# Optimization experiments

Hardware: AMD Instinct MI355X
Metric: run time of the kernel (lower is better)

## Reference

```python
import jax, jax.numpy as jnp
import numpy as np

# ---- config (mirrors init_kwargs) ----
T = 1024          # num tokens (one causal sequence)
H = 1024          # hidden_size
NQ, NK, D = 16, 4, 64   # q heads, kv heads, head_dim (GQA)
I_DENSE = 4096    # dense FFN intermediate
I_MOE = 512       # expert FFN intermediate
E, K = 8, 2       # num_experts, top_k
EPS = 1e-6
THETA = 10000.0


def setup_inputs() -> dict:
    key = jax.random.key(0)
    ks = jax.random.split(key, 20)
    rn = lambda k, shp: (jax.random.normal(k, shp, dtype=jnp.float32) * 0.02)
    QKV = (NQ + 2 * NK) * D
    return {
        "hidden_states": jax.random.normal(ks[0], (T, H), dtype=jnp.float32),
        "residual": jax.random.normal(ks[1], (T, H), dtype=jnp.float32),
        "positions": jnp.arange(T, dtype=jnp.int32),
        "ln0_w": jnp.ones((H,), jnp.float32),
        "pa0_w": jnp.ones((H,), jnp.float32),
        "ln1_w": jnp.ones((H,), jnp.float32),
        "pa1_w": jnp.ones((H,), jnp.float32),
        # attention weights (stored [in, out] so x @ W)
        "qkv0_w": rn(ks[2], (H, QKV)),
        "o0_w": rn(ks[3], (NQ * D, H)),
        "qkv1_w": rn(ks[4], (H, QKV)),
        "o1_w": rn(ks[5], (NQ * D, H)),
        # dense MLPs (merged gate_up: first half gate, second half up)
        "gu0_w": rn(ks[6], (H, 2 * I_DENSE)),
        "dn0_w": rn(ks[7], (I_DENSE, H)),
        "gu1_w": rn(ks[8], (H, 2 * I_DENSE)),
        "dn1_w": rn(ks[9], (I_DENSE, H)),
        # MoE: router gate + per-expert SwiGLU weights
        "gate_w": rn(ks[10], (H, E)),
        "w13": rn(ks[11], (E, H, 2 * I_MOE)),
        "w2": rn(ks[12], (E, I_MOE, H)),
    }


def _rmsnorm(x, w):
    v = jnp.mean(jnp.square(x.astype(jnp.float32)), axis=-1, keepdims=True)
    return (x.astype(jnp.float32) * jax.lax.rsqrt(v + EPS)).astype(x.dtype) * w


def _add_rmsnorm(x, res, w):
    # sglang fused add + RMSNorm: residual <- x + residual; out <- rmsnorm(residual)
    res = x + res
    return _rmsnorm(res, w), res


def _rope(pos, x):
    # neox-style rotary over full head_dim; x: [T, n_heads, D]
    half = D // 2
    inv_freq = 1.0 / (THETA ** (jnp.arange(half, dtype=jnp.float32) / half))
    f = pos.astype(jnp.float32)[:, None] * inv_freq            # [T, half]
    cos, sin = jnp.cos(f)[:, None, :], jnp.sin(f)[:, None, :]  # [T, 1, half]
    x1, x2 = x[..., :half], x[..., half:]
    return jnp.concatenate([x1 * cos - x2 * sin, x2 * cos + x1 * sin], axis=-1)


def _attention(pos, x, qkv_w, o_w):
    qkv = x @ qkv_w
    q = qkv[:, : NQ * D].reshape(T, NQ, D)
    k = qkv[:, NQ * D : (NQ + NK) * D].reshape(T, NK, D)
    v = qkv[:, (NQ + NK) * D :].reshape(T, NK, D)
    q, k = _rope(pos, q), _rope(pos, k)
    g = NQ // NK
    qg = q.reshape(T, NK, g, D)
    scores = jnp.einsum("tkgd,skd->kgts", qg, k) * (D ** -0.5)  # [NK,g,T,T]
    causal = jnp.tril(jnp.ones((T, T), bool))
    scores = jnp.where(causal, scores, jnp.float32(-1e30))
    p = jax.nn.softmax(scores, axis=-1)
    o = jnp.einsum("kgts,skd->tkgd", p, v).reshape(T, NQ * D)
    return o @ o_w


def _dense_mlp(x, gu_w, dn_w):
    gu = x @ gu_w
    h = jax.nn.silu(gu[:, :I_DENSE]) * gu[:, I_DENSE:]  # SiluAndMul
    return h @ dn_w


def _moe(x, gate_w, w13, w2):
    # router in fp32 (router_dtype == 'float32'), softmax, top-k, no renormalize
    logits = x.astype(jnp.float32) @ gate_w.astype(jnp.float32)  # [T, E]
    probs = jax.nn.softmax(logits, axis=-1)
    topw, topi = jax.lax.top_k(probs, K)                         # [T, K]
    rows = jnp.arange(x.shape[0])[:, None]
    combine = jnp.zeros((x.shape[0], E), jnp.float32).at[rows, topi].set(topw)
    combine = combine.astype(x.dtype)
    out = jnp.zeros_like(x)
    for e in range(E):  # fixed small expert count: grouped-GEMM reference
        g = x @ w13[e]
        h = jax.nn.silu(g[:, :I_MOE]) * g[:, I_MOE:]
        out = out + combine[:, e : e + 1] * (h @ w2[e])
    return out


def reference(hidden_states, residual, positions, ln0_w, pa0_w, ln1_w, pa1_w,
              qkv0_w, o0_w, qkv1_w, o1_w, gu0_w, dn0_w, gu1_w, dn1_w,
              gate_w, w13, w2):
    h, r = _add_rmsnorm(hidden_states, residual, ln0_w)
    h = _attention(positions, h, qkv0_w, o0_w)
    h, r = _add_rmsnorm(h, r, pa0_w)
    shortcut = _moe(h, gate_w, w13, w2)      # MoE runs on the shortcut branch
    h = _dense_mlp(h, gu0_w, dn0_w)
    h, r = _add_rmsnorm(h, r, ln1_w)
    h = _attention(positions, h, qkv1_w, o1_w)
    h, r = _add_rmsnorm(h, r, pa1_w)
    h = _dense_mlp(h, gu1_w, dn1_w)
    h = h + shortcut                          # combine shortcut MoE output
    return h, r
```

## Files before the change

### kernel.cpp

```cpp
#include <hip/hip_runtime.h>
#include <math.h>

namespace {

constexpr int kT = 1024;
constexpr int kH = 1024;
constexpr int kNQ = 16;
constexpr int kNKV = 4;
constexpr int kD = 64;
constexpr int kQKV = (kNQ + 2 * kNKV) * kD;
constexpr int kIDense = 4096;
constexpr int kIMoe = 512;
constexpr int kE = 8;
constexpr float kEps = 1e-6f;

typedef __attribute__((ext_vector_type(8))) short short8;
typedef __attribute__((ext_vector_type(4))) float f32x4;

__device__ __forceinline__ ushort f2bf(float f) {
    union { float f; uint32_t u; } v; v.f = f;
    uint32_t r = (v.u + 0x7fffu + ((v.u >> 16) & 1u)) >> 16;
    return (ushort)r;
}
__device__ __forceinline__ float f4el(const float4& v, int i) {
    return (i == 0) ? v.x : (i == 1) ? v.y : (i == 2) ? v.z : v.w;
}
__device__ __forceinline__ void gload16(const void* g, void* l) {
    __builtin_amdgcn_global_load_lds(
        (const __attribute__((address_space(1))) void*)g,
        (__attribute__((address_space(3))) void*)l, 16, 0, 0);
}

__global__ __launch_bounds__(256) void add_rmsnorm_kernel(
    const float* __restrict__ x, const float* __restrict__ res,
    const float* __restrict__ w, float* __restrict__ h32,
    ushort* __restrict__ h16, float* __restrict__ r_out)
{
    __shared__ float red[4];
    const int t = blockIdx.x;
    const int i = threadIdx.x;
    const size_t base = (size_t)t * kH;
    float4 a = reinterpret_cast<const float4*>(x + base)[i];
    float4 b = reinterpret_cast<const float4*>(res + base)[i];
    float4 s = make_float4(a.x + b.x, a.y + b.y, a.z + b.z, a.w + b.w);
    reinterpret_cast<float4*>(r_out + base)[i] = s;
    float ss = s.x * s.x + s.y * s.y + s.z * s.z + s.w * s.w;
    #pragma unroll
    for (int off = 32; off > 0; off >>= 1) ss += __shfl_down(ss, off);
    if ((i & 63) == 0) red[i >> 6] = ss;
    __syncthreads();
    const float tot = red[0] + red[1] + red[2] + red[3];
    const float inv = rsqrtf(tot * (1.0f / kH) + kEps);
    float4 wv = reinterpret_cast<const float4*>(w)[i];
    float4 o = make_float4(s.x * inv * wv.x, s.y * inv * wv.y,
                           s.z * inv * wv.z, s.w * inv * wv.w);
    reinterpret_cast<float4*>(h32 + base)[i] = o;
    ushort4 u;
    u.x = f2bf(o.x); u.y = f2bf(o.y); u.z = f2bf(o.z); u.w = f2bf(o.w);
    reinterpret_cast<ushort4*>(h16 + base)[i] = u;
}

__global__ __launch_bounds__(256) void transpose_bf16_kernel(
    const float* __restrict__ W, ushort* __restrict__ WT,
    int R, int Cn, int ld_w, long w_z_stride, long wt_z_stride)
{
    __shared__ float tile[64][65];
    const int z = blockIdx.z;
    const float* Wz = W + (size_t)z * w_z_stride;
    ushort* WTz = WT + (size_t)z * wt_z_stride;
    const int r0 = blockIdx.y * 64;
    const int c0 = blockIdx.x * 64;
    const int tr = threadIdx.x >> 4;
    const int tc4 = (threadIdx.x & 15) * 4;
    #pragma unroll
    for (int p = 0; p < 4; p++) {
        float4 v = *reinterpret_cast<const float4*>(
            &Wz[(size_t)(r0 + p * 16 + tr) * ld_w + c0 + tc4]);
        tile[p * 16 + tr][tc4 + 0] = v.x;
        tile[p * 16 + tr][tc4 + 1] = v.y;
        tile[p * 16 + tr][tc4 + 2] = v.z;
        tile[p * 16 + tr][tc4 + 3] = v.w;
    }
    __syncthreads();
    #pragma unroll
    for (int p = 0; p < 4; p++) {
        const int oc = p * 16 + tr;
        ushort4 u;
        u.x = f2bf(tile[tc4 + 0][oc]);
        u.y = f2bf(tile[tc4 + 1][oc]);
        u.z = f2bf(tile[tc4 + 2][oc]);
        u.w = f2bf(tile[tc4 + 3][oc]);
        *reinterpret_cast<ushort4*>(&WTz[(size_t)(c0 + oc) * R + r0 + tc4]) = u;
    }
}

template <bool GATED>
__global__ __launch_bounds__(256) void mgemm_kernel(
    const ushort* __restrict__ A, const float* __restrict__ B,
    float* __restrict__ Cf, ushort* __restrict__ C16,
    const float* __restrict__ scale,
    int lda, int ldb, int ldc, int kc,
    int gate_off_cols, long b_z_stride, int c_z_col, int k_z_off,
    int scale_stride, int atomic_flag)
{
    __shared__ __align__(16) ushort As[64 * 64];
    __shared__ __align__(16) ushort Bs[64 * 72];
    __shared__ __align__(16) ushort Us[GATED ? 64 * 72 : 8];

    const int z = blockIdx.z;
    const int m0 = blockIdx.y * 64;
    const int n0 = blockIdx.x * 64;
    const int tid = threadIdx.x;
    const float* Bz = B + (size_t)z * b_z_stride;
    const int k0 = z * k_z_off;

    const int arow = tid >> 3;
    const int achk = tid & 7;
    const int bt = tid & 15;
    const int bq = tid >> 4;

    const int lane = tid & 63;
    const int wave = tid >> 6;
    const int wr = (wave >> 1) * 32;
    const int wc = (wave & 1) * 32;
    const int lrow = lane & 15;
    const int lg = lane >> 4;

    f32x4 accg[2][2] = {};
    f32x4 accu[2][2] = {};

    for (int kk0 = 0; kk0 < kc; kk0 += 64) {
        const int kbase = k0 + kk0;
        #pragma unroll
        for (int c = 0; c < 2; c++) {
            const int row = c * 32 + arow;
            const int cs = (achk + (row & 7)) & 7;
            gload16(A + (size_t)(m0 + row) * lda + kbase + cs * 8,
                    (char*)As + c * 4096 + tid * 16);
        }
        #pragma unroll
        for (int p = 0; p < 2; p++) {
            const int kp = bq + p * 16;
            const long krow = (long)(kbase + kp * 2) * ldb + n0 + bt * 4;
            float4 b0 = *reinterpret_cast<const float4*>(Bz + krow);
            float4 b1 = *reinterpret_cast<const float4*>(Bz + krow + ldb);
            float4 u0, u1;
            if constexpr (GATED) {
                u0 = *reinterpret_cast<const float4*>(Bz + krow + gate_off_cols);
                u1 = *reinterpret_cast<const float4*>(Bz + krow + ldb + gate_off_cols);
            }
            #pragma unroll
            for (int i = 0; i < 4; i++) {
                const int n = bt * 4 + i;
                const int ld = (kp + 4 * ((n >> 2) & 7)) & 31;
                uint32_t pk = (uint32_t)f2bf(f4el(b0, i)) |
                              ((uint32_t)f2bf(f4el(b1, i)) << 16);
                *reinterpret_cast<uint32_t*>(&Bs[n * 72 + ld * 2]) = pk;
                if constexpr (GATED) {
                    uint32_t pu = (uint32_t)f2bf(f4el(u0, i)) |
                                  ((uint32_t)f2bf(f4el(u1, i)) << 16);
                    *reinterpret_cast<uint32_t*>(&Us[n * 72 + ld * 2]) = pu;
                }
            }
        }
        __syncthreads();

        short8 af[2][2], bfr[2][2];
        #pragma unroll
        for (int mf = 0; mf < 2; mf++)
            #pragma unroll
            for (int kk = 0; kk < 2; kk++) {
                const int r = wr + mf * 16 + lrow;
                const int ch = kk * 4 + lg;
                const int sl = (ch - (r & 7)) & 7;
                af[mf][kk] = *reinterpret_cast<const short8*>(
                    (const char*)As + r * 128 + sl * 16);
            }
        #pragma unroll
        for (int nf = 0; nf < 2; nf++)
            #pragma unroll
            for (int kk = 0; kk < 2; kk++) {
                const int n = wc + nf * 16 + lrow;
                const int ldd = ((kk * 16 + lg * 4) + 4 * ((n >> 2) & 7)) & 31;
                bfr[nf][kk] = *reinterpret_cast<const short8*>(&Bs[n * 72 + ldd * 2]);
            }
        #pragma unroll
        for (int mf = 0; mf < 2; mf++)
            #pragma unroll
            for (int nf = 0; nf < 2; nf++)
                #pragma unroll
                for (int kk = 0; kk < 2; kk++)
                    accg[mf][nf] = __builtin_amdgcn_mfma_f32_16x16x32_bf16(
                        af[mf][kk], bfr[nf][kk], accg[mf][nf], 0, 0, 0);
        if constexpr (GATED) {
            short8 uf[2][2];
            #pragma unroll
            for (int nf = 0; nf < 2; nf++)
                #pragma unroll
                for (int kk = 0; kk < 2; kk++) {
                    const int n = wc + nf * 16 + lrow;
                    const int ldd = ((kk * 16 + lg * 4) + 4 * ((n >> 2) & 7)) & 31;
                    uf[nf][kk] = *reinterpret_cast<const short8*>(&Us[n * 72 + ldd * 2]);
                }
            #pragma unroll
            for (int mf = 0; mf < 2; mf++)
                #pragma unroll
                for (int nf = 0; nf < 2; nf++)
                    #pragma unroll
                    for (int kk = 0; kk < 2; kk++)
                        accu[mf][nf] = __builtin_amdgcn_mfma_f32_16x16x32_bf16(
                            af[mf][kk], uf[nf][kk], accu[mf][nf], 0, 0, 0);
        }
        __syncthreads();
    }

    const int r4 = (lane >> 4) * 4;
    const int cl = lane & 15;
    const int ccol = z * c_z_col;
    #pragma unroll
    for (int mf = 0; mf < 2; mf++) {
        #pragma unroll
        for (int nf = 0; nf < 2; nf++) {
            #pragma unroll
            for (int j = 0; j < 4; j++) {
                const int row = m0 + wr + mf * 16 + r4 + j;
                const int col = ccol + n0 + wc + nf * 16 + cl;
                if constexpr (GATED) {
                    const float g = accg[mf][nf][j];
                    const float u = accu[mf][nf][j];
                    const float sv =
                        scale ? scale[(size_t)row * scale_stride + z] : 1.0f;
                    const float h = (g / (1.0f + __expf(-g))) * u * sv;
                    C16[(size_t)row * ldc + col] = f2bf(h);
                } else if (atomic_flag) {
                    atomicAdd(&Cf[(size_t)row * ldc + col], accg[mf][nf][j]);
                } else {
                    Cf[(size_t)row * ldc + col] = accg[mf][nf][j];
                }
            }
        }
    }
}

__global__ __launch_bounds__(256) void rope_pack_kernel(
    const float* __restrict__ qkv, const int* __restrict__ positions,
    ushort* __restrict__ Qb, ushort* __restrict__ Kb)
{
    const int t = blockIdx.x;
    const float pos = (float)positions[t];
    for (int item = threadIdx.x; item < (kNQ + kNKV) * 32; item += 256) {
        const int head = item >> 5;
        const int i = item & 31;
        const float inv_freq = powf(10000.0f, -(float)i * (1.0f / 32.0f));
        const float f = pos * inv_freq;
        float sv, cv;
        sincosf(f, &sv, &cv);
        const size_t off = (size_t)t * kQKV + head * kD;
        const float x1 = qkv[off + i];
        const float x2 = qkv[off + 32 + i];
        const float r1 = x1 * cv - x2 * sv;
        const float r2 = x2 * cv + x1 * sv;
        if (head < kNQ) {
            ushort* q = Qb + ((size_t)head * kT + t) * kD;
            q[i] = f2bf(r1 * 0.125f);
            q[i + 32] = f2bf(r2 * 0.125f);
        } else {
            ushort* k = Kb + ((size_t)(head - kNQ) * kT + t) * kD;
            k[i] = f2bf(r1);
            k[i + 32] = f2bf(r2);
        }
    }
}

__global__ __launch_bounds__(64) void gate_topk_kernel(
    const float* __restrict__ h, const float* __restrict__ gate_w,
    float* __restrict__ combine)
{
    const int t = blockIdx.x;
    const int lane = threadIdx.x;
    float acc[kE] = {};
    for (int i = lane; i < kH; i += 64) {
        const float xv = h[(size_t)t * kH + i];
        const float* gw = gate_w + (size_t)i * kE;
        #pragma unroll
        for (int e = 0; e < kE; e++) acc[e] += xv * gw[e];
    }
    #pragma unroll
    for (int e = 0; e < kE; e++) {
        #pragma unroll
        for (int off = 32; off > 0; off >>= 1) acc[e] += __shfl_down(acc[e], off);
    }
    if (lane == 0) {
        float mx = acc[0];
        #pragma unroll
        for (int e = 1; e < kE; e++) mx = fmaxf(mx, acc[e]);
        float p[kE];
        float s = 0.0f;
        #pragma unroll
        for (int e = 0; e < kE; e++) { p[e] = expf(acc[e] - mx); s += p[e]; }
        const float invs = 1.0f / s;
        #pragma unroll
        for (int e = 0; e < kE; e++) p[e] *= invs;
        int i1 = 0;
        #pragma unroll
        for (int e = 1; e < kE; e++) if (p[e] > p[i1]) i1 = e;
        int i2 = (i1 == 0) ? 1 : 0;
        #pragma unroll
        for (int e = 0; e < kE; e++) if (e != i1 && p[e] > p[i2]) i2 = e;
        float outv[kE];
        #pragma unroll
        for (int e = 0; e < kE; e++) outv[e] = 0.0f;
        outv[i1] = p[i1];
        outv[i2] = p[i2];
        #pragma unroll
        for (int e = 0; e < kE; e++) combine[(size_t)t * kE + e] = outv[e];
    }
}

__global__ __launch_bounds__(256) void attn_mfma_kernel(
    const ushort* __restrict__ Qb, const ushort* __restrict__ Kb,
    const ushort* __restrict__ Vt, ushort* __restrict__ attn_o)
{
    __shared__ __align__(16) ushort Qs[64 * 64];
    __shared__ __align__(16) ushort Ks[64 * 64];
    __shared__ __align__(16) ushort Vs[64 * 64];
    __shared__ __align__(16) ushort Ps[64 * 64];
    const int tid = threadIdx.x;
    const int qb = blockIdx.x * 64;
    const int hq = blockIdx.y;
    const int kvh = hq >> 2;
    const int lane = tid & 63;
    const int wave = tid >> 6;
    const int lrow = lane & 15;
    const int g = lane >> 4;
    const int srow = tid >> 3;
    const int sx = tid & 7;
    const ushort* Qg = Qb + ((size_t)hq * kT + qb) * kD;
    const ushort* Kg = Kb + (size_t)kvh * kT * kD;
    const ushort* Vg = Vt + (size_t)kvh * kD * kT;
    const int xr = (lrow & 7) << 4;

    #pragma unroll
    for (int c = 0; c < 2; c++) {
        const int row = c * 32 + srow;
        gload16(Qg + (size_t)row * kD + ((sx ^ (row & 7)) * 8),
                (char*)Qs + c * 4096 + tid * 16);
    }
    __syncthreads();
    short8 qf[2];
    #pragma unroll
    for (int kk = 0; kk < 2; kk++)
        qf[kk] = *reinterpret_cast<const short8*>(
            (const char*)Qs + (16 * wave + lrow) * 128 + ((kk * 64 + g * 16) ^ xr));

    f32x4 oacc[4] = {};
    float mrow = -1e30f, lsum = 0.0f;

    for (int s0 = 0; s0 <= qb; s0 += 64) {
        __syncthreads();
        #pragma unroll
        for (int c = 0; c < 2; c++) {
            const int row = c * 32 + srow;
            gload16(Kg + (size_t)(s0 + row) * kD + ((sx ^ (row & 7)) * 8),
                    (char*)Ks + c * 4096 + tid * 16);
            gload16(Vg + (size_t)row * kT + s0 + ((sx ^ (row & 7)) * 8),
                    (char*)Vs + c * 4096 + tid * 16);
        }
        __syncthreads();

        f32x4 sacc[4] = {};
        #pragma unroll
        for (int nf = 0; nf < 4; nf++) {
            #pragma unroll
            for (int kk = 0; kk < 2; kk++) {
                short8 kf = *reinterpret_cast<const short8*>(
                    (const char*)Ks + (nf * 16 + lrow) * 128 + ((kk * 64 + g * 16) ^ xr));
                sacc[nf] = __builtin_amdgcn_mfma_f32_16x16x32_bf16(
                    kf, qf[kk], sacc[nf], 0, 0, 0);
            }
        }

        const bool diag = (s0 == qb);
        float pv[16];
        float mloc = -1e30f;
        #pragma unroll
        for (int nf = 0; nf < 4; nf++)
            #pragma unroll
            for (int j = 0; j < 4; j++) {
                float s = sacc[nf][j];
                if (diag && (nf * 16 + g * 4 + j > 16 * wave + lrow)) s = -1e30f;
                pv[nf * 4 + j] = s;
                mloc = fmaxf(mloc, s);
            }
        mloc = fmaxf(mloc, __shfl_xor(mloc, 16));
        mloc = fmaxf(mloc, __shfl_xor(mloc, 32));
        const float mnew = fmaxf(mrow, mloc);
        const float alpha = __expf(mrow - mnew);
        float psum = 0.0f;
        #pragma unroll
        for (int j = 0; j < 16; j++) { pv[j] = __expf(pv[j] - mnew); psum += pv[j]; }
        psum += __shfl_xor(psum, 16);
        psum += __shfl_xor(psum, 32);
        lsum = lsum * alpha + psum;
        mrow = mnew;

        const int prow = 16 * wave + lrow;
        #pragma unroll
        for (int nf = 0; nf < 4; nf++)
            #pragma unroll
            for (int jp = 0; jp < 2; jp++) {
                uint32_t pk = (uint32_t)f2bf(pv[nf * 4 + jp * 2]) |
                              ((uint32_t)f2bf(pv[nf * 4 + jp * 2 + 1]) << 16);
                *reinterpret_cast<uint32_t*>(
                    (char*)Ps + prow * 128 + ((nf * 32 + g * 8 + jp * 4) ^ xr)) = pk;
            }

        float aj[4];
        #pragma unroll
        for (int j = 0; j < 4; j++) aj[j] = __shfl(alpha, g * 4 + j);
        #pragma unroll
        for (int nf = 0; nf < 4; nf++)
            #pragma unroll
            for (int j = 0; j < 4; j++) oacc[nf][j] *= aj[j];

        short8 paf[2];
        #pragma unroll
        for (int kk = 0; kk < 2; kk++)
            paf[kk] = *reinterpret_cast<const short8*>(
                (const char*)Ps + prow * 128 + ((kk * 64 + g * 16) ^ xr));
        #pragma unroll
        for (int nf = 0; nf < 4; nf++)
            #pragma unroll
            for (int kk = 0; kk < 2; kk++) {
                short8 vf = *reinterpret_cast<const short8*>(
                    (const char*)Vs + (nf * 16 + lrow) * 128 + ((kk * 64 + g * 16) ^ xr));
                oacc[nf] = __builtin_amdgcn_mfma_f32_16x16x32_bf16(
                    paf[kk], vf, oacc[nf], 0, 0, 0);
            }
    }

    float lj[4];
    #pragma unroll
    for (int j = 0; j < 4; j++) lj[j] = 1.0f / __shfl(lsum, g * 4 + j);
    #pragma unroll
    for (int nf = 0; nf < 4; nf++)
        #pragma unroll
        for (int j = 0; j < 4; j++) {
            const int trow = qb + 16 * wave + g * 4 + j;
            attn_o[(size_t)trow * (kNQ * kD) + hq * kD + nf * 16 + lrow] =
                f2bf(oacc[nf][j] * lj[j]);
        }
}

__global__ __launch_bounds__(256) void final_out_kernel(
    const float* __restrict__ mlp, const float* __restrict__ shortcut,
    const float* __restrict__ r, float* __restrict__ out)
{
    const int i = blockIdx.x * 256 + threadIdx.x;
    float4 a = reinterpret_cast<const float4*>(mlp)[i];
    float4 b = reinterpret_cast<const float4*>(shortcut)[i];
    reinterpret_cast<float4*>(out)[i] =
        make_float4(a.x + b.x, a.y + b.y, a.z + b.z, a.w + b.w);
    reinterpret_cast<float4*>(out + (size_t)kT * kH)[i] =
        reinterpret_cast<const float4*>(r)[i];
}

}

extern "C" void kernel_launch(void* const* d_in, const int* in_sizes, int n_in,
                              void* d_out, int out_size, void* d_ws, size_t ws_size,
                              hipStream_t stream) {
    (void)in_sizes; (void)n_in; (void)out_size; (void)ws_size;
    const float* hidden   = (const float*)d_in[0];
    const float* residual = (const float*)d_in[1];
    const int*   positions= (const int*)d_in[2];
    const float* ln0_w    = (const float*)d_in[3];
    const float* pa0_w    = (const float*)d_in[4];
    const float* ln1_w    = (const float*)d_in[5];
    const float* pa1_w    = (const float*)d_in[6];
    const float* qkv0_w   = (const float*)d_in[7];
    const float* o0_w     = (const float*)d_in[8];
    const float* qkv1_w   = (const float*)d_in[9];
    const float* o1_w     = (const float*)d_in[10];
    const float* gu0_w    = (const float*)d_in[11];
    const float* dn0_w    = (const float*)d_in[12];
    const float* gu1_w    = (const float*)d_in[13];
    const float* dn1_w    = (const float*)d_in[14];
    const float* gate_w   = (const float*)d_in[15];
    const float* w13      = (const float*)d_in[16];
    const float* w2       = (const float*)d_in[17];
    float* out_h = (float*)d_out;

    char* wsb = (char*)d_ws;
    float*  r_buf   = (float*)(wsb + (0ull  << 20));
    float*  h32     = (float*)(wsb + (4ull  << 20));
    float*  t0_buf  = (float*)(wsb + (8ull  << 20));
    float*  qkv_buf = (float*)(wsb + (12ull << 20));
    float*  sc_buf  = (float*)(wsb + (18ull << 20));
    float*  cb_buf  = (float*)(wsb + (22ull << 20));
    ushort* h16     = (ushort*)(wsb + (23ull << 20));
    ushort* ao16    = (ushort*)(wsb + (25ull << 20));
    ushort* he16    = (ushort*)(wsb + (27ull << 20));
    ushort* Qb      = (ushort*)(wsb + (35ull << 20));
    ushort* Kb      = (ushort*)(wsb + (37ull << 20));
    ushort* VtG     = (ushort*)(wsb + (38ull << 20));

    auto gemm_f32 = [&](const ushort* A, const float* B, float* C, int N,
                        int lda_, int ldb_, int ldc_, int nz, int kc, int kzoff,
                        int atomic) {
        mgemm_kernel<false><<<dim3(N / 64, kT / 64, nz), 256, 0, stream>>>(
            A, B, C, nullptr, nullptr, lda_, ldb_, ldc_, kc,
            0, 0, 0, kzoff, 0, atomic);
    };
    auto attention = [&](const float* qkv_w, const float* o_w) {
        gemm_f32(h16, qkv_w, qkv_buf, kQKV, kH, kQKV, kQKV, 1, kH, 0, 0);
        rope_pack_kernel<<<kT, 256, 0, stream>>>(qkv_buf, positions, Qb, Kb);
        transpose_bf16_kernel<<<dim3(1, kT / 64, kNKV), 256, 0, stream>>>(
            qkv_buf + (kNQ + kNKV) * kD, VtG, kT, kD, kQKV, kD, (long)kD * kT);
        attn_mfma_kernel<<<dim3(kT / 64, kNQ), 256, 0, stream>>>(Qb, Kb, VtG, ao16);
        hipMemsetAsync(t0_buf, 0, (size_t)kT * kH * 4, stream);
        gemm_f32(ao16, o_w, t0_buf, kH, kNQ * kD, kH, kH, 2, 512, 512, 1);
    };
    auto dense_mlp = [&](const float* gu_w, const float* dn_w) {
        mgemm_kernel<true><<<dim3(kIDense / 64, kT / 64, 1), 256, 0, stream>>>(
            h16, gu_w, nullptr, he16, nullptr, kH, 2 * kIDense, kIDense, kH,
            kIDense, 0, 0, 0, 0, 0);
        hipMemsetAsync(t0_buf, 0, (size_t)kT * kH * 4, stream);
        gemm_f32(he16, dn_w, t0_buf, kH, kIDense, kH, kH, 4, 1024, 1024, 1);
    };

    add_rmsnorm_kernel<<<kT, 256, 0, stream>>>(hidden, residual, ln0_w, h32, h16, r_buf);
    attention(qkv0_w, o0_w);
    add_rmsnorm_kernel<<<kT, 256, 0, stream>>>(t0_buf, r_buf, pa0_w, h32, h16, r_buf);
    gate_topk_kernel<<<kT, 64, 0, stream>>>(h32, gate_w, cb_buf);
    mgemm_kernel<true><<<dim3(kIMoe / 64, kT / 64, kE), 256, 0, stream>>>(
        h16, w13, nullptr, he16, cb_buf, kH, 2 * kIMoe, kIDense, kH,
        kIMoe, (long)kH * 2 * kIMoe, kIMoe, 0, kE, 0);
    hipMemsetAsync(sc_buf, 0, (size_t)kT * kH * 4, stream);
    gemm_f32(he16, w2, sc_buf, kH, kIDense, kH, kH, 4, 1024, 1024, 1);
    dense_mlp(gu0_w, dn0_w);
    add_rmsnorm_kernel<<<kT, 256, 0, stream>>>(t0_buf, r_buf, ln1_w, h32, h16, r_buf);
    attention(qkv1_w, o1_w);
    add_rmsnorm_kernel<<<kT, 256, 0, stream>>>(t0_buf, r_buf, pa1_w, h32, h16, r_buf);
    dense_mlp(gu1_w, dn1_w);
    final_out_kernel<<<(kT * kH / 4) / 256, 256, 0, stream>>>(t0_buf, sc_buf, r_buf, out_h);
}
```

Measured before the change: 390.5 us.

## Double-buffer shared-memory tiles in mgemm to overlap loads with MFMA

Shared-memory A/B/U tiles in the GEMM kernel are now double-buffered. The next K-tile's A async load and B global loads into registers are issued before the current tile's MFMAs, and the B conversion is written to the alternate buffer afterwards. This hides global-load latency behind compute and drops one barrier per iteration. In exchange it doubles LDS use, which may lower occupancy, and adds register pressure from holding B prefetch data across the MFMA section.

```diff
diff --git a/kernel.cpp b/kernel.cpp
--- a/kernel.cpp
+++ b/kernel.cpp
@@ -103,9 +103,9 @@
     int gate_off_cols, long b_z_stride, int c_z_col, int k_z_off,
     int scale_stride, int atomic_flag)
 {
-    __shared__ __align__(16) ushort As[64 * 64];
-    __shared__ __align__(16) ushort Bs[64 * 72];
-    __shared__ __align__(16) ushort Us[GATED ? 64 * 72 : 8];
+    __shared__ __align__(16) ushort As[2][64 * 64];
+    __shared__ __align__(16) ushort Bs[2][64 * 72];
+    __shared__ __align__(16) ushort Us[GATED ? 2 : 1][GATED ? 64 * 72 : 8];
 
     const int z = blockIdx.z;
     const int m0 = blockIdx.y * 64;
@@ -113,6 +113,7 @@
     const int tid = threadIdx.x;
     const float* Bz = B + (size_t)z * b_z_stride;
     const int k0 = z * k_z_off;
+    const int nt = kc >> 6;
 
     const int arow = tid >> 3;
     const int achk = tid & 7;
@@ -128,42 +129,61 @@
 
     f32x4 accg[2][2] = {};
     f32x4 accu[2][2] = {};
-
-    for (int kk0 = 0; kk0 < kc; kk0 += 64) {
-        const int kbase = k0 + kk0;
+    float4 rb0[2], rb1[2], ru0[2], ru1[2];
+
+    auto issueA = [&](int t, int buf) {
+        const int kbase = k0 + t * 64;
         #pragma unroll
         for (int c = 0; c < 2; c++) {
             const int row = c * 32 + arow;
             const int cs = (achk + (row & 7)) & 7;
             gload16(A + (size_t)(m0 + row) * lda + kbase + cs * 8,
-                    (char*)As + c * 4096 + tid * 16);
-        }
+                    (char*)As[buf] + c * 4096 + tid * 16);
+        }
+    };
+    auto loadB = [&](int t) {
+        const int kbase = k0 + t * 64;
         #pragma unroll
         for (int p = 0; p < 2; p++) {
             const int kp = bq + p * 16;
             const long krow = (long)(kbase + kp * 2) * ldb + n0 + bt * 4;
-            float4 b0 = *reinterpret_cast<const float4*>(Bz + krow);
-            float4 b1 = *reinterpret_cast<const float4*>(Bz + krow + ldb);
-            float4 u0, u1;
+            rb0[p] = *reinterpret_cast<const float4*>(Bz + krow);
+            rb1[p] = *reinterpret_cast<const float4*>(Bz + krow + ldb);
             if constexpr (GATED) {
-                u0 = *reinterpret_cast<const float4*>(Bz + krow + gate_off_cols);
-                u1 = *reinterpret_cast<const float4*>(Bz + krow + ldb + gate_off_cols);
-            }
+                ru0[p] = *reinterpret_cast<const float4*>(Bz + krow + gate_off_cols);
+                ru1[p] = *reinterpret_cast<const float4*>(Bz + krow + ldb + gate_off_cols);
+            }
+        }
+    };
+    auto writeB = [&](int buf) {
+        #pragma unroll
+        for (int p = 0; p < 2; p++) {
+            const int kp = bq + p * 16;
             #pragma unroll
             for (int i = 0; i < 4; i++) {
                 const int n = bt * 4 + i;
                 const int ld = (kp + 4 * ((n >> 2) & 7)) & 31;
-                uint32_t pk = (uint32_t)f2bf(f4el(b0, i)) |
-                              ((uint32_t)f2bf(f4el(b1, i)) << 16);
-                *reinterpret_cast<uint32_t*>(&Bs[n * 72 + ld * 2]) = pk;
+                uint32_t pk = (uint32_t)f2bf(f4el(rb0[p], i)) |
+                              ((uint32_t)f2bf(f4el(rb1[p], i)) << 16);
+                *reinterpret_cast<uint32_t*>(&Bs[buf][n * 72 + ld * 2]) = pk;
                 if constexpr (GATED) {
-                    uint32_t pu = (uint32_t)f2bf(f4el(u0, i)) |
-                                  ((uint32_t)f2bf(f4el(u1, i)) << 16);
-                    *reinterpret_cast<uint32_t*>(&Us[n * 72 + ld * 2]) = pu;
+                    uint32_t pu = (uint32_t)f2bf(f4el(ru0[p], i)) |
+                                  ((uint32_t)f2bf(f4el(ru1[p], i)) << 16);
+                    *reinterpret_cast<uint32_t*>(&Us[buf][n * 72 + ld * 2]) = pu;
                 }
             }
         }
-        __syncthreads();
+    };
+
+    issueA(0, 0);
+    loadB(0);
+    writeB(0);
+    __syncthreads();
+
+    for (int t = 0; t < nt; ++t) {
+        const int cur = t & 1;
+        const bool more = (t + 1 < nt);
+        if (more) { issueA(t + 1, cur ^ 1); loadB(t + 1); }
 
         short8 af[2][2], bfr[2][2];
         #pragma unroll
@@ -174,7 +194,7 @@
                 const int ch = kk * 4 + lg;
                 const int sl = (ch - (r & 7)) & 7;
                 af[mf][kk] = *reinterpret_cast<const short8*>(
-                    (const char*)As + r * 128 + sl * 16);
+                    (const char*)As[cur] + r * 128 + sl * 16);
             }
         #pragma unroll
         for (int nf = 0; nf < 2; nf++)
@@ -182,7 +202,7 @@
             for (int kk = 0; kk < 2; kk++) {
                 const int n = wc + nf * 16 + lrow;
                 const int ldd = ((kk * 16 + lg * 4) + 4 * ((n >> 2) & 7)) & 31;
-                bfr[nf][kk] = *reinterpret_cast<const short8*>(&Bs[n * 72 + ldd * 2]);
+                bfr[nf][kk] = *reinterpret_cast<const short8*>(&Bs[cur][n * 72 + ldd * 2]);
             }
         #pragma unroll
         for (int mf = 0; mf < 2; mf++)
@@ -200,7 +220,7 @@
                 for (int kk = 0; kk < 2; kk++) {
                     const int n = wc + nf * 16 + lrow;
                     const int ldd = ((kk * 16 + lg * 4) + 4 * ((n >> 2) & 7)) & 31;
-                    uf[nf][kk] = *reinterpret_cast<const short8*>(&Us[n * 72 + ldd * 2]);
+                    uf[nf][kk] = *reinterpret_cast<const short8*>(&Us[cur][n * 72 + ldd * 2]);
                 }
             #pragma unroll
             for (int mf = 0; mf < 2; mf++)
@@ -211,6 +231,8 @@
                         accu[mf][nf] = __builtin_amdgcn_mfma_f32_16x16x32_bf16(
                             af[mf][kk], uf[nf][kk], accu[mf][nf], 0, 0, 0);
         }
+
+        if (more) writeB(cur ^ 1);
         __syncthreads();
     }
 
```

Measured after the change: 409.6 us. 1.05x slower.
